# Kernel tuning notes

Hardware: AMD Instinct MI355X
Metric: run time of the kernel (lower is better)

## Reference

```python
import jax, jax.numpy as jnp
import numpy as np

# quantization formats
E_Q, M_Q = 4, 3      # E4M3 fp8 for input/param quantizers
E_A, M_A = 5, 10     # fp16-like accumulate / output format


def quant(x, exp, man):
    """Round-to-nearest-even float quantization to (exp, man) bits,
    with subnormals and saturation (mptorch float_quantize semantics)."""
    ebias = 2 ** (exp - 1) - 1
    emin = 1 - ebias                      # min normal exponent
    maxv = (2.0 - 2.0 ** (-man)) * 2.0 ** ebias
    ax = jnp.abs(x)
    e = jnp.floor(jnp.log2(jnp.where(ax > 0, ax, 1.0)))
    e = jnp.maximum(e, emin)              # subnormal range shares emin scale
    scale = jnp.exp2(man - e)
    q = jnp.round(x * scale) / scale      # jnp.round is half-to-even
    return jnp.clip(q, -maxv, maxv)


def qgemm(x, wt, exp_add, man_add):
    """Custom-precision GEMM x[M,K] @ wt[K,N] with fma=True:
    the running accumulator is requantized to (exp_add, man_add)
    after every rank-1 (per-k) fused multiply-add."""
    M, K = x.shape
    N = wt.shape[1]

    def step(acc, xw):
        xk, wk = xw                       # [M], [N]
        acc = quant(acc + xk[:, None] * wk[None, :], exp_add, man_add)
        return acc, None

    acc0 = jnp.zeros((M, N), x.dtype)
    acc, _ = jax.lax.scan(step, acc0, (x.T, wt))
    return acc


def setup_inputs() -> dict:
    key = jax.random.key(0)
    k1, k2, k3 = jax.random.split(key, 3)
    in_f, out_f, m = 1024, 1024, 2048
    x = jax.random.normal(k1, (m, in_f), jnp.float32)
    weight = jax.random.normal(k2, (out_f, in_f), jnp.float32) / np.float32(np.sqrt(in_f))
    bound = 1.0 / np.float32(np.sqrt(in_f))
    bias = jax.random.uniform(k3, (out_f,), jnp.float32, -bound, bound)
    return {"x": x, "weight": weight, "bias": bias}


def reference(x, weight, bias):
    qx = quant(x, E_Q, M_Q)               # input_quant
    qw = quant(weight, E_Q, M_Q)          # param_quant
    qb = quant(bias, E_Q, M_Q)            # param_quant
    out = qgemm(qx, qw.T, E_A, M_A)       # float_gemm with fma accumulation
    out = out + qb[None, :]
    out = quant(out, E_A, M_A)            # output requantization
    return out
```

## Files before the change

kernel.cpp:

```cpp
#include <hip/hip_runtime.h>
#include <hip/hip_fp16.h>


#define M_DIM 2048
#define N_DIM 1024
#define K_DIM 1024

#define BM 32
#define BN 128
#define BK 64

__device__ __forceinline__ float quant_e4m3(float v) {
  unsigned au = __float_as_uint(v) & 0x7fffffffu;
  if (au == 0u) return v;
  int e = (int)(au >> 23) - 127;
  if (e < -6) e = -6;
  float s  = __uint_as_float((unsigned)(130 - e) << 23);
  float is = __uint_as_float((unsigned)(124 + e) << 23);
  float r = rintf(v * s) * is;
  return fminf(240.f, fmaxf(-240.f, r));
}

__global__ __launch_bounds__(256) void qt_kernel(const float* __restrict__ in,
                                                 __half* __restrict__ outp,
                                                 int R, int C) {
  __shared__ float tile[32][33];
  const int tx = threadIdx.x & 31;
  const int ty = threadIdx.x >> 5;
  const int c0 = blockIdx.x * 32;
  const int r0 = blockIdx.y * 32;
#pragma unroll
  for (int i = 0; i < 4; i++) {
    int r = r0 + ty + i * 8;
    tile[ty + i * 8][tx] = quant_e4m3(in[(size_t)r * C + c0 + tx]);
  }
  __syncthreads();
#pragma unroll
  for (int i = 0; i < 4; i++) {
    int c = c0 + ty + i * 8;
    outp[(size_t)c * R + r0 + tx] = __float2half(tile[tx][ty + i * 8]);
  }
}

__global__ __launch_bounds__(256) void qbias_kernel(const float* __restrict__ b,
                                                    float* __restrict__ qb) {
  int i = blockIdx.x * 256 + threadIdx.x;
  qb[i] = quant_e4m3(b[i]);
}

__global__ __launch_bounds__(256, 2) void gemm_qfma(const __half* __restrict__ xT,
                                                    const __half* __restrict__ wT,
                                                    const float* __restrict__ qb,
                                                    float* __restrict__ outp) {
  __shared__ unsigned xs[BK][BM];
  __shared__ unsigned wsh[BK][BN / 2];
  const int tid = threadIdx.x;
  const int tn = tid & 31;
  const int tm = tid >> 5;
  const int bn0 = blockIdx.x * BN;
  const int bm0 = blockIdx.y * BM;

  __half2 acc[4][2];
#pragma unroll
  for (int i = 0; i < 4; i++)
#pragma unroll
    for (int j = 0; j < 2; j++) acc[i][j] = __float2half2_rn(0.0f);

  const int xr = tid >> 2;
  const int xc = (tid & 3) << 3;
  const int wc = (tid & 15) << 3;
  const int wr = tid >> 4;

  for (int kc = 0; kc < K_DIM; kc += BK) {
    __syncthreads();
    {
      uint4 v = *reinterpret_cast<const uint4*>(xT + (size_t)(kc + xr) * M_DIM + bm0 + xc);
      unsigned* d = &xs[xr][xc];
      d[0] = (v.x & 0xffffu) * 0x10001u;
      d[1] = (v.x >> 16)     * 0x10001u;
      d[2] = (v.y & 0xffffu) * 0x10001u;
      d[3] = (v.y >> 16)     * 0x10001u;
      d[4] = (v.z & 0xffffu) * 0x10001u;
      d[5] = (v.z >> 16)     * 0x10001u;
      d[6] = (v.w & 0xffffu) * 0x10001u;
      d[7] = (v.w >> 16)     * 0x10001u;
    }
#pragma unroll
    for (int p = 0; p < 4; p++) {
      const int r = wr + (p << 4);
      *reinterpret_cast<uint4*>(&wsh[r][wc >> 1]) =
          *reinterpret_cast<const uint4*>(wT + (size_t)(kc + r) * N_DIM + bn0 + wc);
    }
    __syncthreads();
#pragma unroll
    for (int kk = 0; kk < BK; kk++) {
      const uint4 xv = *reinterpret_cast<const uint4*>(&xs[kk][tm << 2]);
      const uint2 wv = *reinterpret_cast<const uint2*>(&wsh[kk][tn << 1]);
      const __half2 w0 = *reinterpret_cast<const __half2*>(&wv.x);
      const __half2 w1 = *reinterpret_cast<const __half2*>(&wv.y);
      const __half2 x0 = *reinterpret_cast<const __half2*>(&xv.x);
      const __half2 x1 = *reinterpret_cast<const __half2*>(&xv.y);
      const __half2 x2 = *reinterpret_cast<const __half2*>(&xv.z);
      const __half2 x3 = *reinterpret_cast<const __half2*>(&xv.w);
      acc[0][0] = __hfma2(x0, w0, acc[0][0]);
      acc[0][1] = __hfma2(x0, w1, acc[0][1]);
      acc[1][0] = __hfma2(x1, w0, acc[1][0]);
      acc[1][1] = __hfma2(x1, w1, acc[1][1]);
      acc[2][0] = __hfma2(x2, w0, acc[2][0]);
      acc[2][1] = __hfma2(x2, w1, acc[2][1]);
      acc[3][0] = __hfma2(x3, w0, acc[3][0]);
      acc[3][1] = __hfma2(x3, w1, acc[3][1]);
    }
  }

  const float4 bv = *reinterpret_cast<const float4*>(qb + bn0 + (tn << 2));
#pragma unroll
  for (int i = 0; i < 4; i++) {
    float4 o;
    o.x = __half2float(__float2half(__low2float(acc[i][0])  + bv.x));
    o.y = __half2float(__float2half(__high2float(acc[i][0]) + bv.y));
    o.z = __half2float(__float2half(__low2float(acc[i][1])  + bv.z));
    o.w = __half2float(__float2half(__high2float(acc[i][1]) + bv.w));
    *reinterpret_cast<float4*>(outp + (size_t)(bm0 + (tm << 2) + i) * N_DIM + bn0 + (tn << 2)) = o;
  }
}

extern "C" void kernel_launch(void* const* d_in, const int* in_sizes, int n_in,
                              void* d_out, int out_size, void* d_ws, size_t ws_size,
                              hipStream_t stream) {
  const float* x = (const float*)d_in[0];
  const float* w = (const float*)d_in[1];
  const float* b = (const float*)d_in[2];
  float* outp = (float*)d_out;

  char* ws = (char*)d_ws;
  __half* xT = (__half*)ws;
  __half* wT = (__half*)(ws + (size_t)(4 << 20));
  float*  qb = (float*)(ws + (size_t)(6 << 20));

  hipLaunchKernelGGL(qt_kernel, dim3(K_DIM / 32, M_DIM / 32), dim3(256), 0, stream,
                     x, xT, M_DIM, K_DIM);
  hipLaunchKernelGGL(qt_kernel, dim3(K_DIM / 32, N_DIM / 32), dim3(256), 0, stream,
                     w, wT, N_DIM, K_DIM);
  hipLaunchKernelGGL(qbias_kernel, dim3(N_DIM / 256), dim3(256), 0, stream, b, qb);
  hipLaunchKernelGGL(gemm_qfma, dim3(N_DIM / BN, M_DIM / BM), dim3(256), 0, stream,
                     xT, wT, qb, outp);
}
```

Baseline: 120.8 us.

## Enlarge GEMM register tile, use op_sel packed FMA, prefetch tiles, fuse prep kernels

Doubles the per-thread output tile to 4x8 halves and BM to 64, and uses inline v_pk_fma_f16 with op_sel to broadcast x halves instead of storing duplicated x in shared memory. Global loads for the next K tile are prefetched into registers while the current tile is computed. The three quantize/transpose prep launches are merged into one kernel. This trades fewer blocks (256 total) and lower occupancy for more reuse per LDS read and less launch overhead.

```diff
diff --git a/kernel.cpp b/kernel.cpp
--- a/kernel.cpp
+++ b/kernel.cpp
@@ -6,9 +6,16 @@
 #define N_DIM 1024
 #define K_DIM 1024
 
-#define BM 32
+#define BM 64
 #define BN 128
 #define BK 64
+
+#define PKFMA_LO(acc, x, w) \
+  asm("v_pk_fma_f16 %0, %1, %2, %0 op_sel:[0,0,0] op_sel_hi:[0,1,1]" \
+      : "+v"(acc) : "v"(x), "v"(w))
+#define PKFMA_HI(acc, x, w) \
+  asm("v_pk_fma_f16 %0, %1, %2, %0 op_sel:[1,0,0] op_sel_hi:[1,1,1]" \
+      : "+v"(acc) : "v"(x), "v"(w))
 
 __device__ __forceinline__ float quant_e4m3(float v) {
   unsigned au = __float_as_uint(v) & 0x7fffffffu;
@@ -21,14 +28,30 @@
   return fminf(240.f, fmaxf(-240.f, r));
 }
 
-__global__ __launch_bounds__(256) void qt_kernel(const float* __restrict__ in,
-                                                 __half* __restrict__ outp,
-                                                 int R, int C) {
+__global__ __launch_bounds__(256) void prep_kernel(const float* __restrict__ x,
+                                                   const float* __restrict__ w,
+                                                   const float* __restrict__ b,
+                                                   __half* __restrict__ xT,
+                                                   __half* __restrict__ wT,
+                                                   float* __restrict__ qb) {
+  const int id = blockIdx.x;
+  if (id == 3072) {
+    int i = threadIdx.x;
+#pragma unroll
+    for (int p = 0; p < 4; p++) qb[i + p * 256] = quant_e4m3(b[i + p * 256]);
+    return;
+  }
+  const float* in;
+  __half* outp;
+  int R, C, bx, by;
+  if (id < 2048) { in = x; outp = xT; R = M_DIM; C = K_DIM; bx = id & 31; by = id >> 5; }
+  else           { in = w; outp = wT; R = N_DIM; C = K_DIM; bx = (id - 2048) & 31; by = (id - 2048) >> 5; }
+
   __shared__ float tile[32][33];
   const int tx = threadIdx.x & 31;
   const int ty = threadIdx.x >> 5;
-  const int c0 = blockIdx.x * 32;
-  const int r0 = blockIdx.y * 32;
+  const int c0 = bx * 32;
+  const int r0 = by * 32;
 #pragma unroll
   for (int i = 0; i < 4; i++) {
     int r = r0 + ty + i * 8;
@@ -42,86 +65,91 @@
   }
 }
 
-__global__ __launch_bounds__(256) void qbias_kernel(const float* __restrict__ b,
-                                                    float* __restrict__ qb) {
-  int i = blockIdx.x * 256 + threadIdx.x;
-  qb[i] = quant_e4m3(b[i]);
-}
+__global__ __launch_bounds__(256) void gemm_qfma(const __half* __restrict__ xT,
+                                                 const __half* __restrict__ wT,
+                                                 const float* __restrict__ qb,
+                                                 float* __restrict__ outp) {
+  __shared__ __half xs[BK][BM];
+  __shared__ __half wsh[BK][BN];
 
-__global__ __launch_bounds__(256, 2) void gemm_qfma(const __half* __restrict__ xT,
-                                                    const __half* __restrict__ wT,
-                                                    const float* __restrict__ qb,
-                                                    float* __restrict__ outp) {
-  __shared__ unsigned xs[BK][BM];
-  __shared__ unsigned wsh[BK][BN / 2];
   const int tid = threadIdx.x;
-  const int tn = tid & 31;
-  const int tm = tid >> 5;
+  const int tn = tid & 15;
+  const int tm = tid >> 4;
   const int bn0 = blockIdx.x * BN;
   const int bm0 = blockIdx.y * BM;
 
-  __half2 acc[4][2];
+  unsigned acc[4][4];
 #pragma unroll
   for (int i = 0; i < 4; i++)
 #pragma unroll
-    for (int j = 0; j < 2; j++) acc[i][j] = __float2half2_rn(0.0f);
+    for (int j = 0; j < 4; j++) acc[i][j] = 0u;
 
-  const int xr = tid >> 2;
-  const int xc = (tid & 3) << 3;
-  const int wc = (tid & 15) << 3;
-  const int wr = tid >> 4;
+  const int xr = tid >> 3, xc = (tid & 7) * 8;
+  const int wr = tid >> 4, wc = (tid & 15) * 8;
+
+  uint4 gx[2], gw[4];
+#pragma unroll
+  for (int p = 0; p < 2; p++)
+    gx[p] = *reinterpret_cast<const uint4*>(xT + (size_t)(xr + p * 32) * M_DIM + bm0 + xc);
+#pragma unroll
+  for (int p = 0; p < 4; p++)
+    gw[p] = *reinterpret_cast<const uint4*>(wT + (size_t)(wr + p * 16) * N_DIM + bn0 + wc);
 
   for (int kc = 0; kc < K_DIM; kc += BK) {
     __syncthreads();
-    {
-      uint4 v = *reinterpret_cast<const uint4*>(xT + (size_t)(kc + xr) * M_DIM + bm0 + xc);
-      unsigned* d = &xs[xr][xc];
-      d[0] = (v.x & 0xffffu) * 0x10001u;
-      d[1] = (v.x >> 16)     * 0x10001u;
-      d[2] = (v.y & 0xffffu) * 0x10001u;
-      d[3] = (v.y >> 16)     * 0x10001u;
-      d[4] = (v.z & 0xffffu) * 0x10001u;
-      d[5] = (v.z >> 16)     * 0x10001u;
-      d[6] = (v.w & 0xffffu) * 0x10001u;
-      d[7] = (v.w >> 16)     * 0x10001u;
+#pragma unroll
+    for (int p = 0; p < 2; p++)
+      *reinterpret_cast<uint4*>(&xs[xr + p * 32][xc]) = gx[p];
+#pragma unroll
+    for (int p = 0; p < 4; p++)
+      *reinterpret_cast<uint4*>(&wsh[wr + p * 16][wc]) = gw[p];
+    __syncthreads();
+
+    if (kc + BK < K_DIM) {
+      const int kn = kc + BK;
+#pragma unroll
+      for (int p = 0; p < 2; p++)
+        gx[p] = *reinterpret_cast<const uint4*>(xT + (size_t)(kn + xr + p * 32) * M_DIM + bm0 + xc);
+#pragma unroll
+      for (int p = 0; p < 4; p++)
+        gw[p] = *reinterpret_cast<const uint4*>(wT + (size_t)(kn + wr + p * 16) * N_DIM + bn0 + wc);
     }
-#pragma unroll
-    for (int p = 0; p < 4; p++) {
-      const int r = wr + (p << 4);
-      *reinterpret_cast<uint4*>(&wsh[r][wc >> 1]) =
-          *reinterpret_cast<const uint4*>(wT + (size_t)(kc + r) * N_DIM + bn0 + wc);
-    }
-    __syncthreads();
+
 #pragma unroll
     for (int kk = 0; kk < BK; kk++) {
-      const uint4 xv = *reinterpret_cast<const uint4*>(&xs[kk][tm << 2]);
-      const uint2 wv = *reinterpret_cast<const uint2*>(&wsh[kk][tn << 1]);
-      const __half2 w0 = *reinterpret_cast<const __half2*>(&wv.x);
-      const __half2 w1 = *reinterpret_cast<const __half2*>(&wv.y);
-      const __half2 x0 = *reinterpret_cast<const __half2*>(&xv.x);
-      const __half2 x1 = *reinterpret_cast<const __half2*>(&xv.y);
-      const __half2 x2 = *reinterpret_cast<const __half2*>(&xv.z);
-      const __half2 x3 = *reinterpret_cast<const __half2*>(&xv.w);
-      acc[0][0] = __hfma2(x0, w0, acc[0][0]);
-      acc[0][1] = __hfma2(x0, w1, acc[0][1]);
-      acc[1][0] = __hfma2(x1, w0, acc[1][0]);
-      acc[1][1] = __hfma2(x1, w1, acc[1][1]);
-      acc[2][0] = __hfma2(x2, w0, acc[2][0]);
-      acc[2][1] = __hfma2(x2, w1, acc[2][1]);
-      acc[3][0] = __hfma2(x3, w0, acc[3][0]);
-      acc[3][1] = __hfma2(x3, w1, acc[3][1]);
+      const uint2 xv = *reinterpret_cast<const uint2*>(&xs[kk][tm * 4]);
+      const uint4 wv = *reinterpret_cast<const uint4*>(&wsh[kk][tn * 8]);
+      PKFMA_LO(acc[0][0], xv.x, wv.x); PKFMA_LO(acc[0][1], xv.x, wv.y);
+      PKFMA_LO(acc[0][2], xv.x, wv.z); PKFMA_LO(acc[0][3], xv.x, wv.w);
+      PKFMA_HI(acc[1][0], xv.x, wv.x); PKFMA_HI(acc[1][1], xv.x, wv.y);
+      PKFMA_HI(acc[1][2], xv.x, wv.z); PKFMA_HI(acc[1][3], xv.x, wv.w);
+      PKFMA_LO(acc[2][0], xv.y, wv.x); PKFMA_LO(acc[2][1], xv.y, wv.y);
+      PKFMA_LO(acc[2][2], xv.y, wv.z); PKFMA_LO(acc[2][3], xv.y, wv.w);
+      PKFMA_HI(acc[3][0], xv.y, wv.x); PKFMA_HI(acc[3][1], xv.y, wv.y);
+      PKFMA_HI(acc[3][2], xv.y, wv.z); PKFMA_HI(acc[3][3], xv.y, wv.w);
     }
   }
 
-  const float4 bv = *reinterpret_cast<const float4*>(qb + bn0 + (tn << 2));
+  const float4 bv0 = *reinterpret_cast<const float4*>(qb + bn0 + tn * 8);
+  const float4 bv1 = *reinterpret_cast<const float4*>(qb + bn0 + tn * 8 + 4);
 #pragma unroll
   for (int i = 0; i < 4; i++) {
-    float4 o;
-    o.x = __half2float(__float2half(__low2float(acc[i][0])  + bv.x));
-    o.y = __half2float(__float2half(__high2float(acc[i][0]) + bv.y));
-    o.z = __half2float(__float2half(__low2float(acc[i][1])  + bv.z));
-    o.w = __half2float(__float2half(__high2float(acc[i][1]) + bv.w));
-    *reinterpret_cast<float4*>(outp + (size_t)(bm0 + (tm << 2) + i) * N_DIM + bn0 + (tn << 2)) = o;
+    float4 o0, o1;
+    __half2 h0 = *reinterpret_cast<__half2*>(&acc[i][0]);
+    __half2 h1 = *reinterpret_cast<__half2*>(&acc[i][1]);
+    __half2 h2 = *reinterpret_cast<__half2*>(&acc[i][2]);
+    __half2 h3 = *reinterpret_cast<__half2*>(&acc[i][3]);
+    o0.x = __half2float(__float2half(__low2float(h0)  + bv0.x));
+    o0.y = __half2float(__float2half(__high2float(h0) + bv0.y));
+    o0.z = __half2float(__float2half(__low2float(h1)  + bv0.z));
+    o0.w = __half2float(__float2half(__high2float(h1) + bv0.w));
+    o1.x = __half2float(__float2half(__low2float(h2)  + bv1.x));
+    o1.y = __half2float(__float2half(__high2float(h2) + bv1.y));
+    o1.z = __half2float(__float2half(__low2float(h3)  + bv1.z));
+    o1.w = __half2float(__float2half(__high2float(h3) + bv1.w));
+    float* row = outp + (size_t)(bm0 + tm * 4 + i) * N_DIM + bn0 + tn * 8;
+    *reinterpret_cast<float4*>(row)     = o0;
+    *reinterpret_cast<float4*>(row + 4) = o1;
   }
 }
 
@@ -138,11 +166,8 @@
   __half* wT = (__half*)(ws + (size_t)(4 << 20));
   float*  qb = (float*)(ws + (size_t)(6 << 20));
 
-  hipLaunchKernelGGL(qt_kernel, dim3(K_DIM / 32, M_DIM / 32), dim3(256), 0, stream,
-                     x, xT, M_DIM, K_DIM);
-  hipLaunchKernelGGL(qt_kernel, dim3(K_DIM / 32, N_DIM / 32), dim3(256), 0, stream,
-                     w, wT, N_DIM, K_DIM);
-  hipLaunchKernelGGL(qbias_kernel, dim3(N_DIM / 256), dim3(256), 0, stream, b, qb);
+  hipLaunchKernelGGL(prep_kernel, dim3(3073), dim3(256), 0, stream,
+                     x, w, b, xT, wT, qb);
   hipLaunchKernelGGL(gemm_qfma, dim3(N_DIM / BN, M_DIM / BM), dim3(256), 0, stream,
                      xT, wT, qb, outp);
 }
```

Measured after the change: 137.4 us. +13.7%, slower.
